# Optimization experiments

Measured on AMD Instinct MI355X. Metric: run time of the kernel, lower is better.

## Reference

```python
import jax, jax.numpy as jnp
import numpy as np


def _gcn_conv(x, W, b, src, dst, num_nodes):
    """PyG GCNConv with default args: add self-loops + symmetric normalization.
    x: [N, F_in], W: [F_in, F_out], b: [F_out], src/dst: [E] (self-loops already included).
    """
    h = x @ W  # [N, F_out]
    # in-degree of destination nodes (counting self-loops)
    ones = jnp.ones_like(dst, dtype=h.dtype)
    deg = jax.ops.segment_sum(ones, dst, num_segments=num_nodes)  # [N]
    dinv = jnp.where(deg > 0, jax.lax.rsqrt(jnp.maximum(deg, 1.0)), 0.0)
    norm = dinv[src] * dinv[dst]  # [E]
    msgs = h[src] * norm[:, None]  # [E, F_out] gather + scale
    out = jax.ops.segment_sum(msgs, dst, num_segments=num_nodes)  # scatter-add
    return out + b


def setup_inputs() -> dict:
    key = jax.random.key(0)
    k1, k2, k3, k4 = jax.random.split(key, 4)
    N, E, F_IN, HID = 100000, 1600000, 128, 64
    x = jax.random.normal(k1, (N, F_IN), dtype=jnp.float32)
    edge_index = jax.random.randint(k2, (2, E), 0, N, dtype=jnp.int64)
    W1 = jax.random.normal(k3, (F_IN, HID), dtype=jnp.float32) * (1.0 / np.sqrt(F_IN))
    b1 = jnp.zeros((HID,), dtype=jnp.float32)
    W2 = jax.random.normal(k4, (HID, 1), dtype=jnp.float32) * (1.0 / np.sqrt(HID))
    b2 = jnp.zeros((1,), dtype=jnp.float32)
    return {"x": x, "edge_index": edge_index, "W1": W1, "b1": b1, "W2": W2, "b2": b2}


def reference(x, edge_index, W1, b1, W2, b2):
    N = x.shape[0]
    # add self-loops (GCNConv default add_self_loops=True)
    loop = jnp.arange(N, dtype=edge_index.dtype)
    src = jnp.concatenate([edge_index[0], loop])
    dst = jnp.concatenate([edge_index[1], loop])
    h = jax.nn.relu(_gcn_conv(x, W1, b1, src, dst, N))
    out = _gcn_conv(h, W2, b2, src, dst, N)
    return out  # [N, 1]
```

## Files before the change

kernel.cpp:

```cpp
#include <hip/hip_runtime.h>
#include <hip/hip_fp16.h>

#define F_IN 128
#define HID  64
#define CAP  96
#define CSHIFT 9
#define CNODES 512
#define NC_MAX 256
#define CCHUNK 4096
#define BCAPC 8960

typedef short s16x8 __attribute__((ext_vector_type(8)));
typedef float f32x4 __attribute__((ext_vector_type(4)));

__device__ inline unsigned short bf16rne(float f) {
    unsigned u = __float_as_uint(f);
    return (unsigned short)((u + 0x7FFFu + ((u >> 16) & 1u)) >> 16);
}
__device__ inline float bf16tof(unsigned short h) {
    return __uint_as_float(((unsigned)h) << 16);
}

__launch_bounds__(256)
__global__ void k_coarse(const int* __restrict__ src, const int* __restrict__ dst,
                         int* __restrict__ acur, int* __restrict__ ent, int E, int nc) {
    __shared__ int s_cnt[NC_MAX];
    __shared__ int s_gb[NC_MAX];
    __shared__ int s_bump[NC_MAX];
    int t = threadIdx.x;
    int e0 = blockIdx.x * CCHUNK;
    int n = E - e0; if (n > CCHUNK) n = CCHUNK;

    for (int i = t; i < nc; i += 256) { s_cnt[i] = 0; s_bump[i] = 0; }
    __syncthreads();
    for (int i = t; i < n; i += 256)
        atomicAdd(&s_cnt[dst[e0 + i] >> CSHIFT], 1);
    __syncthreads();
    if (t < nc) {
        int c = s_cnt[t];
        s_gb[t] = (c > 0) ? atomicAdd(&acur[t], c) : 0;
    }
    __syncthreads();
    for (int i = t; i < n; i += 256) {
        int d = dst[e0 + i], s = src[e0 + i];
        int b = d >> CSHIFT;
        int p = s_gb[b] + atomicAdd(&s_bump[b], 1);
        if (p < BCAPC) ent[(size_t)b * BCAPC + p] = (s << CSHIFT) | (d & (CNODES - 1));
    }
}

__launch_bounds__(1024)
__global__ void k_fillc(const int* __restrict__ acur, const int* __restrict__ ent,
                        int* __restrict__ counts, int* __restrict__ csrc, int N) {
    __shared__ int lcnt[CNODES];
    int b = blockIdx.x, t = threadIdx.x;
    if (t < CNODES) lcnt[t] = 0;
    __syncthreads();
    int base = b * CNODES;
    int cnt = acur[b]; if (cnt > BCAPC) cnt = BCAPC;
    const int* ep = ent + (size_t)b * BCAPC;
    for (int i = t; i < cnt; i += 1024) {
        int v = ep[i];
        int ld = v & (CNODES - 1), s = v >> CSHIFT;
        int p = atomicAdd(&lcnt[ld], 1);
        if (p < CAP) csrc[(size_t)(base + ld) * CAP + p] = s;
    }
    __syncthreads();
    if (t < CNODES && base + t < N) {
        int cc = lcnt[t]; if (cc > CAP) cc = CAP;
        counts[base + t] = cc;
    }
}

__launch_bounds__(256)
__global__ void k_wsplit(const float* __restrict__ W1, unsigned short* __restrict__ W1hT,
                         unsigned short* __restrict__ W1lT) {
    int id = blockIdx.x * 256 + threadIdx.x;
    int k = id >> 6, c = id & 63;
    float f = W1[id];
    unsigned short h = bf16rne(f);
    unsigned short l = bf16rne(f - bf16tof(h));
    W1hT[c * F_IN + k] = h;
    W1lT[c * F_IN + k] = l;
}

__launch_bounds__(256)
__global__ void k_gemm(const float* __restrict__ x,
                       const unsigned short* __restrict__ W1hT,
                       const unsigned short* __restrict__ W1lT,
                       const int* __restrict__ counts, __half* __restrict__ hn, int N) {
    int t = threadIdx.x;
    int lane = t & 63;
    int wid = t >> 6;
    int r0w = blockIdx.x * 64 + wid * 16;
    int arow = r0w + (lane & 15);
    int ar = (arow < N) ? arow : (N - 1);
    int kq = lane >> 4;

    const float* xr = x + (size_t)ar * F_IN + kq * 8;
    int coff = (lane & 15) * F_IN + kq * 8;

    f32x4 acc[4];
#pragma unroll
    for (int nt = 0; nt < 4; ++nt) acc[nt] = (f32x4){0.f, 0.f, 0.f, 0.f};

#pragma unroll
    for (int kt = 0; kt < 4; ++kt) {
        float4 xa = *(const float4*)(xr + kt * 32);
        float4 xb = *(const float4*)(xr + kt * 32 + 4);
        float xf[8] = {xa.x, xa.y, xa.z, xa.w, xb.x, xb.y, xb.z, xb.w};
        s16x8 ah, al;
#pragma unroll
        for (int j = 0; j < 8; ++j) {
            unsigned short h = bf16rne(xf[j]);
            ah[j] = (short)h;
            al[j] = (short)bf16rne(xf[j] - bf16tof(h));
        }
        int kb = coff + kt * 32;
#pragma unroll
        for (int nt = 0; nt < 4; ++nt) {
            s16x8 bh = *(const s16x8*)(W1hT + nt * 16 * F_IN + kb);
            s16x8 bl = *(const s16x8*)(W1lT + nt * 16 * F_IN + kb);
            acc[nt] = __builtin_amdgcn_mfma_f32_16x16x32_bf16(ah, bh, acc[nt], 0, 0, 0);
            acc[nt] = __builtin_amdgcn_mfma_f32_16x16x32_bf16(al, bh, acc[nt], 0, 0, 0);
            acc[nt] = __builtin_amdgcn_mfma_f32_16x16x32_bf16(ah, bl, acc[nt], 0, 0, 0);
            acc[nt] = __builtin_amdgcn_mfma_f32_16x16x32_bf16(al, bl, acc[nt], 0, 0, 0);
        }
    }

    int rbase = r0w + (lane >> 4) * 4;
    if (rbase >= N) return;
    int4 c4 = *(const int4*)(counts + rbase);
    int cj[4] = {c4.x, c4.y, c4.z, c4.w};
#pragma unroll
    for (int j = 0; j < 4; ++j) {
        int row = rbase + j;
        if (row < N) {
            float di = rsqrtf((float)(cj[j] + 1));
            __half* hp = hn + (size_t)row * HID + (lane & 15);
#pragma unroll
            for (int nt = 0; nt < 4; ++nt)
                hp[nt * 16] = __float2half_rn(acc[nt][j] * di);
        }
    }
}

__device__ inline void accum8(float acc[8], int4 raw, float w) {
    int v[4] = { raw.x, raw.y, raw.z, raw.w };
#pragma unroll
    for (int h = 0; h < 4; ++h) {
        __half2 h2 = *(__half2*)&v[h];
        float2 f = __half22float2(h2);
        acc[2 * h]     = fmaf(w, f.x, acc[2 * h]);
        acc[2 * h + 1] = fmaf(w, f.y, acc[2 * h + 1]);
    }
}

__launch_bounds__(256)
__global__ void k_gather1(const int* __restrict__ csrc, const int* __restrict__ counts,
                          const __half* __restrict__ hn, const float* __restrict__ b1,
                          const float* __restrict__ W2, float* __restrict__ zn, int N) {
    int lane = threadIdx.x & 63;
    int g    = (lane >> 3) & 3;
    int li   = lane & 7;
    int r = blockIdx.x * 8 + ((threadIdx.x >> 6) << 1) + (lane >> 5);
    int rr = (r < N) ? r : (N - 1);
    int cnt = (r < N) ? counts[rr] : 0;

    const int4* cs4 = (const int4*)(csrc + (size_t)rr * CAP);
    size_t lo = (size_t)li * 8;

    float acc[8];
#pragma unroll
    for (int c = 0; c < 8; ++c) acc[c] = 0.f;

    {
        int4 sA = cs4[g];
        int idx[4]; float w[4];
        idx[0] = sA.x; idx[1] = sA.y; idx[2] = sA.z; idx[3] = sA.w;
#pragma unroll
        for (int k = 0; k < 4; ++k) {
            int e = 4 * g + k;
            bool v = (e < cnt);
            idx[k] = v ? idx[k] : rr;
            w[k]   = v ? 1.f : 0.f;
        }
        int4 raw[4];
#pragma unroll
        for (int k = 0; k < 4; ++k)
            raw[k] = *(const int4*)&hn[(size_t)idx[k] * HID + lo];
#pragma unroll
        for (int k = 0; k < 4; ++k) accum8(acc, raw[k], w[k]);
    }

    int cntO = __shfl_xor(cnt, 32, 64);
    int cmax = (cnt > cntO) ? cnt : cntO;

    if (cmax > 16) {
        int4 sB = cs4[4 + g];
        int idx[4]; float w[4];
        idx[0] = sB.x; idx[1] = sB.y; idx[2] = sB.z; idx[3] = sB.w;
#pragma unroll
        for (int k = 0; k < 4; ++k) {
            int e = 16 + 4 * g + k;
            bool v = (e < cnt);
            idx[k] = v ? idx[k] : rr;
            w[k]   = v ? 1.f : 0.f;
        }
        int4 raw[4];
#pragma unroll
        for (int k = 0; k < 4; ++k)
            raw[k] = *(const int4*)&hn[(size_t)idx[k] * HID + lo];
#pragma unroll
        for (int k = 0; k < 4; ++k) accum8(acc, raw[k], w[k]);
    }

    for (int c = 32; c < cmax; c += 16) {
        int4 s = cs4[(c >> 2) + g];
        int idx[4]; float w[4];
        idx[0] = s.x; idx[1] = s.y; idx[2] = s.z; idx[3] = s.w;
#pragma unroll
        for (int k = 0; k < 4; ++k) {
            int e = c + 4 * g + k;
            bool v = (e < cnt);
            idx[k] = v ? idx[k] : rr;
            w[k]   = v ? 1.f : 0.f;
        }
        int4 raw[4];
#pragma unroll
        for (int k = 0; k < 4; ++k)
            raw[k] = *(const int4*)&hn[(size_t)idx[k] * HID + lo];
#pragma unroll
        for (int k = 0; k < 4; ++k) accum8(acc, raw[k], w[k]);
    }

#pragma unroll
    for (int c = 0; c < 8; ++c) {
        acc[c] += __shfl_xor(acc[c], 8, 64);
        acc[c] += __shfl_xor(acc[c], 16, 64);
    }

    int4 rawR = *(const int4*)&hn[(size_t)rr * HID + lo];
    accum8(acc, rawR, 1.f);

    float di = rsqrtf((float)(cnt + 1));
    float4 b0 = *(const float4*)&b1[li * 8];
    float4 b4 = *(const float4*)&b1[li * 8 + 4];
    float4 w0 = *(const float4*)&W2[li * 8];
    float4 w4 = *(const float4*)&W2[li * 8 + 4];

    float p = fmaxf(fmaf(di, acc[0], b0.x), 0.f) * w0.x
            + fmaxf(fmaf(di, acc[1], b0.y), 0.f) * w0.y
            + fmaxf(fmaf(di, acc[2], b0.z), 0.f) * w0.z
            + fmaxf(fmaf(di, acc[3], b0.w), 0.f) * w0.w
            + fmaxf(fmaf(di, acc[4], b4.x), 0.f) * w4.x
            + fmaxf(fmaf(di, acc[5], b4.y), 0.f) * w4.y
            + fmaxf(fmaf(di, acc[6], b4.z), 0.f) * w4.z
            + fmaxf(fmaf(di, acc[7], b4.w), 0.f) * w4.w;

    p += __shfl_xor(p, 1, 64);
    p += __shfl_xor(p, 2, 64);
    p += __shfl_xor(p, 4, 64);

    if ((lane & 31) == 0 && r < N) zn[r] = p * di;
}

__global__ void k_gather2(const int* __restrict__ csrc, const int* __restrict__ counts,
                          const float* __restrict__ zn, const float* __restrict__ b2,
                          float* __restrict__ out, int N) {
    int t = blockIdx.x * blockDim.x + threadIdx.x;
    int r = t >> 4, li = t & 15;
    if (r >= N) return;
    size_t beg = (size_t)r * CAP;
    int cnt = counts[r];
    float acc = 0.f;
    for (int j = li; j < cnt; j += 16) {
        acc += zn[csrc[beg + j]];
    }
    acc += __shfl_xor(acc, 1, 64);
    acc += __shfl_xor(acc, 2, 64);
    acc += __shfl_xor(acc, 4, 64);
    acc += __shfl_xor(acc, 8, 64);
    if (li == 0) {
        float di = rsqrtf((float)(cnt + 1));
        out[r] = di * (acc + zn[r]) + b2[0];
    }
}

extern "C" void kernel_launch(void* const* d_in, const int* in_sizes, int n_in,
                              void* d_out, int out_size, void* d_ws, size_t ws_size,
                              hipStream_t stream) {
    const float* x  = (const float*)d_in[0];
    const int*   ei = (const int*)d_in[1];
    const float* W1 = (const float*)d_in[2];
    const float* b1 = (const float*)d_in[3];
    const float* W2 = (const float*)d_in[4];
    const float* b2 = (const float*)d_in[5];
    float* out = (float*)d_out;

    const int N = in_sizes[0] / F_IN;
    const int E = in_sizes[1] / 2;
    const int* src = ei;
    const int* dst = ei + E;

    const int nc = (N + CNODES - 1) / CNODES;
    const int NBKT = (N + 63) / 64;

    char* ws = (char*)d_ws;
    size_t off = 0;
    auto alloc = [&](size_t bytes) { void* p = ws + off; off += (bytes + 255) & ~255ULL; return p; };
    int*    acur   = (int*)   alloc((size_t)nc * 4);
    int*    counts = (int*)   alloc((size_t)N * 4);
    float*  zn     = (float*) alloc((size_t)N * 4);
    unsigned short* W1hT = (unsigned short*) alloc((size_t)HID * F_IN * 2);
    unsigned short* W1lT = (unsigned short*) alloc((size_t)HID * F_IN * 2);
    int*    ent    = (int*)   alloc((size_t)nc * BCAPC * 4);
    __half* hn     = (__half*)alloc((size_t)N * HID * 2);
    int*    csrc   = (int*)   alloc((size_t)N * CAP * 4);

    hipMemsetAsync(acur, 0, (size_t)nc * 4, stream);

    const int coarseBlks = (E + CCHUNK - 1) / CCHUNK;
    k_wsplit<<<32, 256, 0, stream>>>(W1, W1hT, W1lT);
    k_coarse<<<coarseBlks, 256, 0, stream>>>(src, dst, acur, ent, E, nc);
    k_fillc<<<nc, 1024, 0, stream>>>(acur, ent, counts, csrc, N);
    k_gemm<<<NBKT, 256, 0, stream>>>(x, W1hT, W1lT, counts, hn, N);
    k_gather1<<<(N + 7) / 8, 256, 0, stream>>>(csrc, counts, hn, b1, W2, zn, N);
    k_gather2<<<((size_t)N * 16 + 255) / 256, 256, 0, stream>>>(csrc, counts, zn, b2, out, N);
}
```

Before: 202.5 us.

## Fold weight split into coarse kernel and stage GEMM x tile via async LDS loads

Moves the W1 bf16 hi/lo split into the first 32 blocks of the coarse bucketing kernel, which removes one kernel launch. Rewrites the GEMM's x loading so that each block copies its 64x128 fp32 tile into shared memory with global_load_lds direct-to-LDS transfers, using an XOR swizzle to avoid bank conflicts. Each lane then reads its fragments from LDS instead of issuing strided global float4 loads. This adds 32KB of LDS per block, which may reduce occupancy. Out-of-range rows are clamped to row 0 of the tile.

```diff
diff --git a/kernel.cpp b/kernel.cpp
--- a/kernel.cpp
+++ b/kernel.cpp
@@ -23,11 +23,24 @@
 
 __launch_bounds__(256)
 __global__ void k_coarse(const int* __restrict__ src, const int* __restrict__ dst,
-                         int* __restrict__ acur, int* __restrict__ ent, int E, int nc) {
+                         int* __restrict__ acur, int* __restrict__ ent, int E, int nc,
+                         const float* __restrict__ W1, unsigned short* __restrict__ W1hT,
+                         unsigned short* __restrict__ W1lT) {
     __shared__ int s_cnt[NC_MAX];
     __shared__ int s_gb[NC_MAX];
     __shared__ int s_bump[NC_MAX];
     int t = threadIdx.x;
+
+    if (blockIdx.x < 32) {
+        int id = blockIdx.x * 256 + t;
+        int k = id >> 6, c = id & 63;
+        float f = W1[id];
+        unsigned short h = bf16rne(f);
+        unsigned short l = bf16rne(f - bf16tof(h));
+        W1hT[c * F_IN + k] = h;
+        W1lT[c * F_IN + k] = l;
+    }
+
     int e0 = blockIdx.x * CCHUNK;
     int n = E - e0; if (n > CCHUNK) n = CCHUNK;
 
@@ -73,32 +86,39 @@
 }
 
 __launch_bounds__(256)
-__global__ void k_wsplit(const float* __restrict__ W1, unsigned short* __restrict__ W1hT,
-                         unsigned short* __restrict__ W1lT) {
-    int id = blockIdx.x * 256 + threadIdx.x;
-    int k = id >> 6, c = id & 63;
-    float f = W1[id];
-    unsigned short h = bf16rne(f);
-    unsigned short l = bf16rne(f - bf16tof(h));
-    W1hT[c * F_IN + k] = h;
-    W1lT[c * F_IN + k] = l;
-}
-
-__launch_bounds__(256)
 __global__ void k_gemm(const float* __restrict__ x,
                        const unsigned short* __restrict__ W1hT,
                        const unsigned short* __restrict__ W1lT,
                        const int* __restrict__ counts, __half* __restrict__ hn, int N) {
+    __shared__ float xs[64 * F_IN];
     int t = threadIdx.x;
     int lane = t & 63;
     int wid = t >> 6;
-    int r0w = blockIdx.x * 64 + wid * 16;
-    int arow = r0w + (lane & 15);
-    int ar = (arow < N) ? arow : (N - 1);
-    int kq = lane >> 4;
-
-    const float* xr = x + (size_t)ar * F_IN + kq * 8;
-    int coff = (lane & 15) * F_IN + kq * 8;
+    int r0 = blockIdx.x * 64;
+
+    const char* gbase = (const char*)(x + (size_t)r0 * F_IN);
+    int rmax = N - r0;
+#pragma unroll
+    for (int c = 0; c < 8; ++c) {
+        int base = (wid * 8 + c) * 1024;
+        int d = base + lane * 16;
+        int soff = d ^ (((d >> 9) & 7) << 4);
+        if ((soff >> 9) >= rmax) soff &= 511;
+        __builtin_amdgcn_global_load_lds(
+            (const __attribute__((address_space(1))) unsigned int*)(gbase + soff),
+            (__attribute__((address_space(3))) unsigned int*)((char*)xs + base),
+            16, 0, 0);
+    }
+    __syncthreads();
+
+    int lr = lane & 15;
+    int q  = lane >> 4;
+    int lrow = wid * 16 + lr;
+    int swz = (lrow & 7) << 4;
+    const char* xrow = (const char*)xs + lrow * 512;
+
+    int r0w = r0 + wid * 16;
+    int coff = lr * F_IN + q * 8;
 
     f32x4 acc[4];
 #pragma unroll
@@ -106,8 +126,9 @@
 
 #pragma unroll
     for (int kt = 0; kt < 4; ++kt) {
-        float4 xa = *(const float4*)(xr + kt * 32);
-        float4 xb = *(const float4*)(xr + kt * 32 + 4);
+        int o  = kt * 128 + q * 32;
+        float4 xa = *(const float4*)(xrow + ((o)      ^ swz));
+        float4 xb = *(const float4*)(xrow + ((o + 16) ^ swz));
         float xf[8] = {xa.x, xa.y, xa.z, xa.w, xb.x, xb.y, xb.z, xb.w};
         s16x8 ah, al;
 #pragma unroll
@@ -128,7 +149,7 @@
         }
     }
 
-    int rbase = r0w + (lane >> 4) * 4;
+    int rbase = r0w + q * 4;
     if (rbase >= N) return;
     int4 c4 = *(const int4*)(counts + rbase);
     int cj[4] = {c4.x, c4.y, c4.z, c4.w};
@@ -137,7 +158,7 @@
         int row = rbase + j;
         if (row < N) {
             float di = rsqrtf((float)(cj[j] + 1));
-            __half* hp = hn + (size_t)row * HID + (lane & 15);
+            __half* hp = hn + (size_t)row * HID + lr;
 #pragma unroll
             for (int nt = 0; nt < 4; ++nt)
                 hp[nt * 16] = __float2half_rn(acc[nt][j] * di);
@@ -321,8 +342,7 @@
     hipMemsetAsync(acur, 0, (size_t)nc * 4, stream);
 
     const int coarseBlks = (E + CCHUNK - 1) / CCHUNK;
-    k_wsplit<<<32, 256, 0, stream>>>(W1, W1hT, W1lT);
-    k_coarse<<<coarseBlks, 256, 0, stream>>>(src, dst, acur, ent, E, nc);
+    k_coarse<<<coarseBlks, 256, 0, stream>>>(src, dst, acur, ent, E, nc, W1, W1hT, W1lT);
     k_fillc<<<nc, 1024, 0, stream>>>(acur, ent, counts, csrc, N);
     k_gemm<<<NBKT, 256, 0, stream>>>(x, W1hT, W1lT, counts, hn, N);
     k_gather1<<<(N + 7) / 8, 256, 0, stream>>>(csrc, counts, hn, b1, W2, zn, N);
```

After: 200.8 us. Within noise of the previous version (-0.8%).

## Replace two-pass bucketed CSR build with single-pass global-atomic scatter

Applied to the files above, without the earlier changes.

Removes the coarse bucketing kernel and the per-bucket fill kernel. In their place, one kernel does a global atomicAdd on per-node counts and writes each source index straight into a fixed-capacity adjacency slot. The gather kernels now clamp counts to CAP, because the raw counts can exceed it. This drops one launch and the intermediate entry buffer, at the cost of contended global atomics and scattered writes to csrc.

```diff
diff --git a/kernel.cpp b/kernel.cpp
--- a/kernel.cpp
+++ b/kernel.cpp
@@ -4,11 +4,6 @@
 #define F_IN 128
 #define HID  64
 #define CAP  96
-#define CSHIFT 9
-#define CNODES 512
-#define NC_MAX 256
-#define CCHUNK 4096
-#define BCAPC 8960
 
 typedef short s16x8 __attribute__((ext_vector_type(8)));
 typedef float f32x4 __attribute__((ext_vector_type(4)));
@@ -21,67 +16,36 @@
     return __uint_as_float(((unsigned)h) << 16);
 }
 
-__launch_bounds__(256)
-__global__ void k_coarse(const int* __restrict__ src, const int* __restrict__ dst,
-                         int* __restrict__ acur, int* __restrict__ ent, int E, int nc) {
-    __shared__ int s_cnt[NC_MAX];
-    __shared__ int s_gb[NC_MAX];
-    __shared__ int s_bump[NC_MAX];
-    int t = threadIdx.x;
-    int e0 = blockIdx.x * CCHUNK;
-    int n = E - e0; if (n > CCHUNK) n = CCHUNK;
-
-    for (int i = t; i < nc; i += 256) { s_cnt[i] = 0; s_bump[i] = 0; }
-    __syncthreads();
-    for (int i = t; i < n; i += 256)
-        atomicAdd(&s_cnt[dst[e0 + i] >> CSHIFT], 1);
-    __syncthreads();
-    if (t < nc) {
-        int c = s_cnt[t];
-        s_gb[t] = (c > 0) ? atomicAdd(&acur[t], c) : 0;
-    }
-    __syncthreads();
-    for (int i = t; i < n; i += 256) {
-        int d = dst[e0 + i], s = src[e0 + i];
-        int b = d >> CSHIFT;
-        int p = s_gb[b] + atomicAdd(&s_bump[b], 1);
-        if (p < BCAPC) ent[(size_t)b * BCAPC + p] = (s << CSHIFT) | (d & (CNODES - 1));
-    }
-}
-
-__launch_bounds__(1024)
-__global__ void k_fillc(const int* __restrict__ acur, const int* __restrict__ ent,
-                        int* __restrict__ counts, int* __restrict__ csrc, int N) {
-    __shared__ int lcnt[CNODES];
-    int b = blockIdx.x, t = threadIdx.x;
-    if (t < CNODES) lcnt[t] = 0;
-    __syncthreads();
-    int base = b * CNODES;
-    int cnt = acur[b]; if (cnt > BCAPC) cnt = BCAPC;
-    const int* ep = ent + (size_t)b * BCAPC;
-    for (int i = t; i < cnt; i += 1024) {
-        int v = ep[i];
-        int ld = v & (CNODES - 1), s = v >> CSHIFT;
-        int p = atomicAdd(&lcnt[ld], 1);
-        if (p < CAP) csrc[(size_t)(base + ld) * CAP + p] = s;
-    }
-    __syncthreads();
-    if (t < CNODES && base + t < N) {
-        int cc = lcnt[t]; if (cc > CAP) cc = CAP;
-        counts[base + t] = cc;
-    }
-}
-
-__launch_bounds__(256)
+__launch_bounds__(512)
 __global__ void k_wsplit(const float* __restrict__ W1, unsigned short* __restrict__ W1hT,
                          unsigned short* __restrict__ W1lT) {
-    int id = blockIdx.x * 256 + threadIdx.x;
+    int id = blockIdx.x * 512 + threadIdx.x;
     int k = id >> 6, c = id & 63;
     float f = W1[id];
     unsigned short h = bf16rne(f);
     unsigned short l = bf16rne(f - bf16tof(h));
     W1hT[c * F_IN + k] = h;
     W1lT[c * F_IN + k] = l;
+}
+
+__launch_bounds__(256)
+__global__ void k_scatter(const int* __restrict__ src, const int* __restrict__ dst,
+                          int* __restrict__ counts, int* __restrict__ csrc, int E) {
+    int base = blockIdx.x * 1024 + threadIdx.x;
+    int d[4], s[4]; bool v[4]; int p[4];
+#pragma unroll
+    for (int k = 0; k < 4; ++k) {
+        int e = base + k * 256;
+        v[k] = (e < E);
+        d[k] = v[k] ? dst[e] : 0;
+        s[k] = v[k] ? src[e] : 0;
+    }
+#pragma unroll
+    for (int k = 0; k < 4; ++k)
+        if (v[k]) p[k] = atomicAdd(&counts[d[k]], 1);
+#pragma unroll
+    for (int k = 0; k < 4; ++k)
+        if (v[k] && p[k] < CAP) csrc[(size_t)d[k] * CAP + p[k]] = s[k];
 }
 
 __launch_bounds__(256)
@@ -166,6 +130,7 @@
     int r = blockIdx.x * 8 + ((threadIdx.x >> 6) << 1) + (lane >> 5);
     int rr = (r < N) ? r : (N - 1);
     int cnt = (r < N) ? counts[rr] : 0;
+    int cw  = (cnt > CAP) ? CAP : cnt;
 
     const int4* cs4 = (const int4*)(csrc + (size_t)rr * CAP);
     size_t lo = (size_t)li * 8;
@@ -181,7 +146,7 @@
 #pragma unroll
         for (int k = 0; k < 4; ++k) {
             int e = 4 * g + k;
-            bool v = (e < cnt);
+            bool v = (e < cw);
             idx[k] = v ? idx[k] : rr;
             w[k]   = v ? 1.f : 0.f;
         }
@@ -193,8 +158,8 @@
         for (int k = 0; k < 4; ++k) accum8(acc, raw[k], w[k]);
     }
 
-    int cntO = __shfl_xor(cnt, 32, 64);
-    int cmax = (cnt > cntO) ? cnt : cntO;
+    int cntO = __shfl_xor(cw, 32, 64);
+    int cmax = (cw > cntO) ? cw : cntO;
 
     if (cmax > 16) {
         int4 sB = cs4[4 + g];
@@ -203,7 +168,7 @@
 #pragma unroll
         for (int k = 0; k < 4; ++k) {
             int e = 16 + 4 * g + k;
-            bool v = (e < cnt);
+            bool v = (e < cw);
             idx[k] = v ? idx[k] : rr;
             w[k]   = v ? 1.f : 0.f;
         }
@@ -222,7 +187,7 @@
 #pragma unroll
         for (int k = 0; k < 4; ++k) {
             int e = c + 4 * g + k;
-            bool v = (e < cnt);
+            bool v = (e < cw);
             idx[k] = v ? idx[k] : rr;
             w[k]   = v ? 1.f : 0.f;
         }
@@ -273,8 +238,9 @@
     if (r >= N) return;
     size_t beg = (size_t)r * CAP;
     int cnt = counts[r];
+    int cw  = (cnt > CAP) ? CAP : cnt;
     float acc = 0.f;
-    for (int j = li; j < cnt; j += 16) {
+    for (int j = li; j < cw; j += 16) {
         acc += zn[csrc[beg + j]];
     }
     acc += __shfl_xor(acc, 1, 64);
@@ -303,27 +269,22 @@
     const int* src = ei;
     const int* dst = ei + E;
 
-    const int nc = (N + CNODES - 1) / CNODES;
     const int NBKT = (N + 63) / 64;
 
     char* ws = (char*)d_ws;
     size_t off = 0;
     auto alloc = [&](size_t bytes) { void* p = ws + off; off += (bytes + 255) & ~255ULL; return p; };
-    int*    acur   = (int*)   alloc((size_t)nc * 4);
-    int*    counts = (int*)   alloc((size_t)N * 4);
+    int*    counts = (int*)   alloc((size_t)N * 4 + 256);
     float*  zn     = (float*) alloc((size_t)N * 4);
     unsigned short* W1hT = (unsigned short*) alloc((size_t)HID * F_IN * 2);
     unsigned short* W1lT = (unsigned short*) alloc((size_t)HID * F_IN * 2);
-    int*    ent    = (int*)   alloc((size_t)nc * BCAPC * 4);
     __half* hn     = (__half*)alloc((size_t)N * HID * 2);
     int*    csrc   = (int*)   alloc((size_t)N * CAP * 4);
 
-    hipMemsetAsync(acur, 0, (size_t)nc * 4, stream);
-
-    const int coarseBlks = (E + CCHUNK - 1) / CCHUNK;
-    k_wsplit<<<32, 256, 0, stream>>>(W1, W1hT, W1lT);
-    k_coarse<<<coarseBlks, 256, 0, stream>>>(src, dst, acur, ent, E, nc);
-    k_fillc<<<nc, 1024, 0, stream>>>(acur, ent, counts, csrc, N);
+    hipMemsetAsync(counts, 0, (size_t)N * 4, stream);
+
+    k_wsplit<<<16, 512, 0, stream>>>(W1, W1hT, W1lT);
+    k_scatter<<<(E + 1023) / 1024, 256, 0, stream>>>(src, dst, counts, csrc, E);
     k_gemm<<<NBKT, 256, 0, stream>>>(x, W1hT, W1lT, counts, hn, N);
     k_gather1<<<(N + 7) / 8, 256, 0, stream>>>(csrc, counts, hn, b1, W2, zn, N);
     k_gather2<<<((size_t)N * 16 + 255) / 256, 256, 0, stream>>>(csrc, counts, zn, b2, out, N);
```

Measured after the change: 284.0 us. 1.4x slower.
